# Performance work log

Hardware: AMD Instinct MI355X
Metric: run time of the kernel (lower is better)

## Reference

```python
import jax, jax.numpy as jnp
import numpy as np
import math

L, E, H, F, V, ML, B, S = 6, 1024, 16, 4096, 1024, 1024, 4, 1024
PAD = V - 1


def setup_inputs() -> dict:
    key = jax.random.key(0)
    ks = jax.random.split(key, 16)
    sc = 0.02
    nrm = lambda k, sh: jax.random.normal(k, sh, jnp.float32) * sc
    return dict(
        sequences=jax.random.randint(ks[0], (B, S), 0, V - 1),
        embed=nrm(ks[1], (V, E)),
        pos_emb=nrm(ks[2], (1, ML + 2, E)),
        dist_emb=nrm(ks[3], (ML + 1, H)),
        in_w=nrm(ks[4], (L, 3 * E, E)), in_b=nrm(ks[5], (L, 3 * E)),
        out_w=nrm(ks[6], (L, E, E)), out_b=nrm(ks[7], (L, E)),
        ln1_g=jnp.ones((L, E)), ln1_b=jnp.zeros((L, E)),
        ff1_w=nrm(ks[8], (L, F, E)), ff1_b=nrm(ks[9], (L, F)),
        ff2_w=nrm(ks[10], (L, E, F)), ff2_b=nrm(ks[11], (L, E)),
        ln2_g=jnp.ones((L, E)), ln2_b=jnp.zeros((L, E)),
        lnf_g=jnp.ones((E,)), lnf_b=jnp.zeros((E,)),
        gen_w=nrm(ks[12], (V, E)), gen_b=jnp.zeros((V,)),
    )


def _layer_norm(h, g, b, eps=1e-5):
    m = h.mean(-1, keepdims=True)
    v = ((h - m) ** 2).mean(-1, keepdims=True)
    return (h - m) * jax.lax.rsqrt(v + eps) * g + b


def reference(sequences, embed, pos_emb, dist_emb, in_w, in_b, out_w, out_b,
              ln1_g, ln1_b, ff1_w, ff1_b, ff2_w, ff2_b, ln2_g, ln2_b,
              lnf_g, lnf_b, gen_w, gen_b):
    b_, s_ = sequences.shape
    dh = E // H
    # token embedding * sqrt(E) + learned positional embedding
    x = embed[sequences] * math.sqrt(E) + pos_emb[:, :s_]  # [B,S,E]
    # relative-distance attention bias, clamped at max_len
    idx = jnp.arange(s_)
    dist = jnp.minimum(jnp.abs(idx[None, :] - idx[:, None]), ML)  # [S,S]
    bias = dist_emb[dist].transpose(2, 0, 1)[None]  # [1,H,S,S]
    causal = idx[None, :] <= idx[:, None]  # lower-triangular allowed
    bias = jnp.where(causal[None, None], bias, -jnp.inf)
    # key padding mask (additive -inf on padded keys)
    kpm = (sequences == PAD)  # [B,S]
    bias = jnp.where(kpm[:, None, None, :], -jnp.inf, bias)  # [B,H,S,S]

    scale = 1.0 / math.sqrt(dh)
    for l in range(L):
        qkv = jnp.einsum('bse,fe->bsf', x, in_w[l]) + in_b[l]
        q, k, v = jnp.split(qkv, 3, axis=-1)
        q = q.reshape(b_, s_, H, dh).transpose(0, 2, 1, 3)
        k = k.reshape(b_, s_, H, dh).transpose(0, 2, 1, 3)
        v = v.reshape(b_, s_, H, dh).transpose(0, 2, 1, 3)
        scores = jnp.einsum('bhqd,bhkd->bhqk', q, k) * scale + bias
        att = jax.nn.softmax(scores, axis=-1)
        ctx = jnp.einsum('bhqk,bhkd->bhqd', att, v)
        ctx = ctx.transpose(0, 2, 1, 3).reshape(b_, s_, E)
        attn_out = jnp.einsum('bse,fe->bsf', ctx, out_w[l]) + out_b[l]
        x = _layer_norm(x + attn_out, ln1_g[l], ln1_b[l])  # post-norm
        h = jax.nn.gelu(jnp.einsum('bse,fe->bsf', x, ff1_w[l]) + ff1_b[l], approximate=False)
        h = jnp.einsum('bsf,ef->bse', h, ff2_w[l]) + ff2_b[l]
        x = _layer_norm(x + h, ln2_g[l], ln2_b[l])
    x = _layer_norm(x, lnf_g, lnf_b)  # final encoder norm
    logits = jnp.einsum('bse,ve->bsv', x, gen_w) + gen_b
    return logits
```

## Files before the change

### kernel.cpp

```cpp
#include <hip/hip_runtime.h>
#include <math.h>
#include <stdint.h>

constexpr int kL = 6;
constexpr int kE = 1024;
constexpr int kH = 16;
constexpr int kF = 4096;
constexpr int kV = 1024;
constexpr int kB = 4;
constexpr int kS = 1024;
constexpr int kRows = kB * kS;

typedef __bf16 bf16_t;
typedef __bf16 bf16x8 __attribute__((ext_vector_type(8)));
typedef __bf16 bf16x4 __attribute__((ext_vector_type(4)));
typedef float f32x4 __attribute__((ext_vector_type(4)));
typedef unsigned int u32x2 __attribute__((ext_vector_type(2)));

#define AS1 __attribute__((address_space(1)))
#define AS3 __attribute__((address_space(3)))

__device__ __forceinline__ void gload_lds16(const void* g, void* l) {
  __builtin_amdgcn_global_load_lds((const AS1 unsigned int*)g, (AS3 unsigned int*)l, 16, 0, 0);
}

__device__ __forceinline__ unsigned lds_u32(const void* p) {
  return (unsigned)(uintptr_t)p;
}

__device__ __forceinline__ float gelu_f(float x) {
  return 0.5f * x * (1.0f + erff(x * 0.70710678118654752440f));
}

template <int CTRL>
__device__ __forceinline__ float dppf(float v) {
  return __builtin_bit_cast(float, __builtin_amdgcn_update_dpp(
      __builtin_bit_cast(int, v), __builtin_bit_cast(int, v), CTRL, 0xF, 0xF, false));
}

__global__ void cast_kernel(const float* __restrict__ in, bf16_t* __restrict__ out, int n4) {
  const int stride = gridDim.x * blockDim.x;
  for (int i = blockIdx.x * blockDim.x + threadIdx.x; i < n4; i += stride) {
    const float4 v = *(const float4*)(in + (size_t)i * 4);
    bf16x4 o;
    o[0] = (bf16_t)v.x; o[1] = (bf16_t)v.y; o[2] = (bf16_t)v.z; o[3] = (bf16_t)v.w;
    *(bf16x4*)(out + (size_t)i * 4) = o;
  }
}

__global__ void embed_kernel(const int* __restrict__ seq, const float* __restrict__ emb,
                             const float* __restrict__ pos, float* __restrict__ x32,
                             bf16_t* __restrict__ xb) {
  const int r = blockIdx.x;
  const int s = r & 1023;
  const int tok = seq[r];
  const int c = threadIdx.x << 2;
  const float4 e = *(const float4*)(emb + (size_t)tok * kE + c);
  const float4 pz = *(const float4*)(pos + (size_t)s * kE + c);
  float4 v;
  v.x = e.x * 32.0f + pz.x;
  v.y = e.y * 32.0f + pz.y;
  v.z = e.z * 32.0f + pz.z;
  v.w = e.w * 32.0f + pz.w;
  *(float4*)(x32 + (size_t)r * kE + c) = v;
  bf16x4 o;
  o[0] = (bf16_t)v.x; o[1] = (bf16_t)v.y; o[2] = (bf16_t)v.z; o[3] = (bf16_t)v.w;
  *(bf16x4*)(xb + (size_t)r * kE + c) = o;
}

template <int MODE>
__global__ void addln_kernel(float* __restrict__ x32, const void* __restrict__ res,
                             const float* __restrict__ gg, const float* __restrict__ bb,
                             bf16_t* __restrict__ xb, const float* __restrict__ bias2) {
  __shared__ float red[8];
  const int r = blockIdx.x;
  const int c = threadIdx.x << 2;
  float4 v = *(const float4*)(x32 + (size_t)r * kE + c);
  if (MODE == 0) {
    const bf16x4 t = *(const bf16x4*)((const bf16_t*)res + (size_t)r * kE + c);
    v.x += (float)t[0]; v.y += (float)t[1]; v.z += (float)t[2]; v.w += (float)t[3];
  }
  if (MODE == 2) {
    const bf16_t* p = (const bf16_t*)res;
#pragma unroll
    for (int part = 0; part < 4; ++part) {
      const bf16x4 t = *(const bf16x4*)(p + (size_t)part * kRows * kE + (size_t)r * kE + c);
      v.x += (float)t[0]; v.y += (float)t[1]; v.z += (float)t[2]; v.w += (float)t[3];
    }
    const float4 b2 = *(const float4*)(bias2 + c);
    v.x += b2.x; v.y += b2.y; v.z += b2.z; v.w += b2.w;
  }
  float s = v.x + v.y + v.z + v.w;
  float q = v.x * v.x + v.y * v.y + v.z * v.z + v.w * v.w;
#pragma unroll
  for (int off = 32; off >= 1; off >>= 1) {
    s += __shfl_xor(s, off, 64);
    q += __shfl_xor(q, off, 64);
  }
  const int w = threadIdx.x >> 6, lane = threadIdx.x & 63;
  if (lane == 0) { red[w] = s; red[4 + w] = q; }
  __syncthreads();
  s = red[0] + red[1] + red[2] + red[3];
  q = red[4] + red[5] + red[6] + red[7];
  const float mean = s * (1.0f / 1024.0f);
  const float var = q * (1.0f / 1024.0f) - mean * mean;
  const float rstd = rsqrtf(var + 1e-5f);
  const float4 g4 = *(const float4*)(gg + c);
  const float4 b4 = *(const float4*)(bb + c);
  float4 o;
  o.x = (v.x - mean) * rstd * g4.x + b4.x;
  o.y = (v.y - mean) * rstd * g4.y + b4.y;
  o.z = (v.z - mean) * rstd * g4.z + b4.z;
  o.w = (v.w - mean) * rstd * g4.w + b4.w;
  if (MODE != 1) *(float4*)(x32 + (size_t)r * kE + c) = o;
  bf16x4 ob;
  ob[0] = (bf16_t)o.x; ob[1] = (bf16_t)o.y; ob[2] = (bf16_t)o.z; ob[3] = (bf16_t)o.w;
  *(bf16x4*)(xb + (size_t)r * kE + c) = ob;
}

template <int EPI>
__launch_bounds__(256, 4)
__global__ void gemm128_kernel(const bf16_t* __restrict__ A, const bf16_t* __restrict__ Bt,
                               const float* __restrict__ bias, void* __restrict__ Cv,
                               int ldA, int ldB, int ldC, int kc, size_t zstride) {
  __shared__ bf16_t lA[64 * 64];
  __shared__ bf16_t lB[64 * 64];
  const int tid = threadIdx.x;
  const int w = tid >> 6;
  const int lane = tid & 63;
  const int g = lane >> 4;
  const int lr = lane & 15;

  const int nwg = gridDim.x * gridDim.y;
  const int lin = blockIdx.y * gridDim.x + blockIdx.x;
  const int cpx = nwg >> 3;
  const int swz = (lin & 7) * cpx + (lin >> 3);
  const int bx = swz % gridDim.x, by = swz / gridDim.x;
  const int bm0 = by << 7;
  const int bn0 = bx << 7;
  const int k0 = blockIdx.z * kc;
  const int wm = (w >> 1) << 6;
  const int wn = (w & 1) << 6;

  const int ln8 = lane >> 3, l8 = lane & 7;
  const int pg = l8 ^ ln8;
  const int arow0 = (w << 5) + (ln8 << 1) + (pg >> 2);
  const int arow1 = arow0 + 16;
  const int kpo = (pg & 3) << 3;
  const bf16_t* srcA0 = A + (size_t)(bm0 + arow0) * ldA + k0 + kpo;
  const bf16_t* srcA1 = A + (size_t)(bm0 + arow1) * ldA + k0 + kpo;
  const bf16_t* srcB0 = Bt + (size_t)(bn0 + arow0) * ldB + k0 + kpo;
  const bf16_t* srcB1 = Bt + (size_t)(bn0 + arow1) * ldB + k0 + kpo;
  bf16_t* dA0 = lA + (w << 10);
  bf16_t* dA1 = lA + (w << 10) + 512;
  bf16_t* dB0 = lB + (w << 10);
  bf16_t* dB1 = lB + (w << 10) + 512;

  f32x4 zz = {0.f, 0.f, 0.f, 0.f};
  f32x4 acc[4][4];
#pragma unroll
  for (int i = 0; i < 4; ++i)
#pragma unroll
    for (int j = 0; j < 4; ++j) acc[i][j] = zz;

  int paoff[4], pboff[4];
#pragma unroll
  for (int i = 0; i < 4; ++i) {
    const int ra = wm + i * 16 + lr;
    paoff[i] = ((ra >> 1) << 6) + (((((ra & 1) << 2) + g) ^ ((ra >> 1) & 7)) << 3);
    const int rb = wn + i * 16 + lr;
    pboff[i] = ((rb >> 1) << 6) + (((((rb & 1) << 2) + g) ^ ((rb >> 1) & 7)) << 3);
  }

  const int NT = kc >> 5;
  for (int t = 0; t < NT; ++t) {
    gload_lds16(srcA0, dA0);
    gload_lds16(srcA1, dA1);
    gload_lds16(srcB0, dB0);
    gload_lds16(srcB1, dB1);
    srcA0 += 32; srcA1 += 32; srcB0 += 32; srcB1 += 32;
    __syncthreads();
    bf16x8 a[4], b[4];
#pragma unroll
    for (int i = 0; i < 4; ++i) a[i] = *(const bf16x8*)&lA[paoff[i]];
#pragma unroll
    for (int i = 0; i < 4; ++i) b[i] = *(const bf16x8*)&lB[pboff[i]];
#pragma unroll
    for (int i = 0; i < 4; ++i)
#pragma unroll
      for (int j = 0; j < 4; ++j)
        acc[i][j] = __builtin_amdgcn_mfma_f32_16x16x32_bf16(a[i], b[j], acc[i][j], 0, 0, 0);
    __syncthreads();
  }

  bf16_t* outb = (bf16_t*)Cv;
  if (EPI == 3) outb += (size_t)blockIdx.z * zstride;
#pragma unroll
  for (int i = 0; i < 4; ++i) {
#pragma unroll
    for (int j = 0; j < 4; ++j) {
      const int col = bn0 + wn + j * 16 + lr;
      float bv = 0.0f;
      if (EPI != 3) bv = bias[col];
#pragma unroll
      for (int rg = 0; rg < 4; ++rg) {
        const int row = bm0 + wm + i * 16 + g * 4 + rg;
        float v = acc[i][j][rg] + bv;
        if (EPI == 2) v = gelu_f(v);
        if (EPI == 1) {
          ((float*)Cv)[(size_t)row * ldC + col] = v;
        } else {
          outb[(size_t)row * ldC + col] = (bf16_t)v;
        }
      }
    }
  }
}

__launch_bounds__(256, 3)
__global__ void attn_kernel(const bf16_t* __restrict__ qkv, const int* __restrict__ seq,
                            const float* __restrict__ dist_emb, bf16_t* __restrict__ ctx) {
  __shared__ float sbias[1024];
  __shared__ unsigned char spad[1024];
  __shared__ bf16_t kbuf[2][64 * 64];
  __shared__ bf16_t vbuf[2][4096];
  __shared__ bf16_t pbuf[4][16][72];
  const int tid = threadIdx.x;
  const int w = tid >> 6, lane = tid & 63, g = lane >> 4, lr = lane & 15;
  const int bid = blockIdx.x;
  const int qt = 15 - (bid >> 6);
  const int h = bid & 15, b = (bid >> 4) & 3;

  const int q0 = qt * 64 + w * 16;
  const bf16_t* qp = qkv + ((size_t)(b * kS + q0 + lr)) * 3072 + h * 64;

  const int p = (w * 64 + lane) * 16;
  const int s_kv = ((p >> 11) << 4) + ((p >> 5) & 15);
  const int s_dv = (((p >> 9) & 3) << 4) + ((p & 31) >> 1);
  const bf16_t* vsrc0 = qkv + ((size_t)(b * kS + s_kv)) * 3072 + 2048 + h * 64 + s_dv;

  const int klrow = (w << 3) + (lane >> 3);
  const int kscol = ((lane & 7) ^ (lane >> 3)) << 3;
  const bf16_t* ksrc0 = qkv + ((size_t)(b * kS + klrow)) * 3072 + 1024 + h * 64 + kscol;

  const int cs0k = (g ^ (lr & 7)) << 3;
  const int cs1k = ((4 + g) ^ (lr & 7)) << 3;

  const int* seqb = seq + b * kS;
  const int nt = qt + 1;

#define STAGEKV(bufi, kt_) {                                                        \
    gload_lds16(ksrc0 + (size_t)((kt_) * 64) * 3072, &kbuf[bufi][(w << 3) * 64]);   \
    gload_lds16(ksrc0 + (size_t)((kt_) * 64 + 32) * 3072,                           \
                &kbuf[bufi][(32 + (w << 3)) * 64]);                                 \
    gload_lds16(vsrc0 + (size_t)((kt_) * 64) * 3072, &vbuf[bufi][w << 9]);          \
    gload_lds16(vsrc0 + (size_t)((kt_) * 64 + 32) * 3072,                           \
                &vbuf[bufi][2048 + (w << 9)]);                                      \
  }

  STAGEKV(0, 0);
  const bf16x8 qf0 = *(const bf16x8*)(qp + g * 8);
  const bf16x8 qf1 = *(const bf16x8*)(qp + 32 + g * 8);
  for (int i = tid; i < 1024; i += 256) {
    sbias[i] = dist_emb[i * kH + h];
    spad[i] = (seqb[i] == kV - 1) ? 1 : 0;
  }

  f32x4 zz = {0.f, 0.f, 0.f, 0.f};
  f32x4 oacc[4];
#pragma unroll
  for (int n = 0; n < 4; ++n) oacc[n] = zz;
  float m_[4], l_[4];
#pragma unroll
  for (int j = 0; j < 4; ++j) { m_[j] = -1e30f; l_[j] = 0.f; }

  __syncthreads();

#define ATT_STEP64(kt_, bz) do {                                                    \
    bf16x8 kf0[4], kf1[4];                                                          \
    _Pragma("unroll")                                                               \
    for (int ns = 0; ns < 4; ++ns) {                                                \
      const int krow = (ns * 16 + lr) * 64;                                         \
      kf0[ns] = *(const bf16x8*)&kbuf[bz][krow + cs0k];                             \
      kf1[ns] = *(const bf16x8*)&kbuf[bz][krow + cs1k];                             \
    }                                                                               \
    f32x4 s_[4];                                                                    \
    _Pragma("unroll")                                                               \
    for (int ns = 0; ns < 4; ++ns) {                                                \
      f32x4 z = zz;                                                                 \
      z = __builtin_amdgcn_mfma_f32_16x16x32_bf16(qf0, kf0[ns], z, 0, 0, 0);        \
      z = __builtin_amdgcn_mfma_f32_16x16x32_bf16(qf1, kf1[ns], z, 0, 0, 0);        \
      s_[ns] = z;                                                                   \
    }                                                                               \
    const int colb = (kt_) * 64 + lr;                                               \
    bool pad[4];                                                                    \
    _Pragma("unroll")                                                               \
    for (int ns = 0; ns < 4; ++ns) pad[ns] = spad[colb + ns * 16] != 0;             \
    float sv[4][4], lmax[4];                                                        \
    _Pragma("unroll")                                                               \
    for (int j = 0; j < 4; ++j) {                                                   \
      const int r = q0 + g * 4 + j;                                                 \
      _Pragma("unroll")                                                             \
      for (int ns = 0; ns < 4; ++ns) {                                              \
        const int cc = colb + ns * 16;                                              \
        sv[ns][j] = (cc <= r && !pad[ns]) ? s_[ns][j] * 0.125f + sbias[r - cc]      \
                                          : -1e30f;                                 \
      }                                                                             \
      lmax[j] = fmaxf(fmaxf(sv[0][j], sv[1][j]), fmaxf(sv[2][j], sv[3][j]));        \
    }                                                                               \
             \
    const bool okk = (lmax[0] <= m_[0] + 8.0f) && (lmax[1] <= m_[1] + 8.0f) &&      \
                     (lmax[2] <= m_[2] + 8.0f) && (lmax[3] <= m_[3] + 8.0f);        \
    if (!__all((int)okk)) {                                                         \
      float mj[4], corr[4];                                                         \
      _Pragma("unroll")                                                             \
      for (int j = 0; j < 4; ++j) {                                                 \
        mj[j] = lmax[j];                                                            \
        mj[j] = fmaxf(mj[j], dppf<0x121>(mj[j]));                                   \
        mj[j] = fmaxf(mj[j], dppf<0x122>(mj[j]));                                   \
        mj[j] = fmaxf(mj[j], dppf<0x124>(mj[j]));                                   \
        mj[j] = fmaxf(mj[j], dppf<0x128>(mj[j]));                                   \
        const float mn = fmaxf(m_[j], mj[j]);                                       \
        corr[j] = __expf(m_[j] - mn);                                               \
        m_[j] = mn;                                                                 \
        l_[j] *= corr[j];                                                           \
      }                                                                             \
      _Pragma("unroll")                                                             \
      for (int n = 0; n < 4; ++n) {                                                 \
        f32x4 t = oacc[n];                                                          \
        t[0] *= corr[0]; t[1] *= corr[1]; t[2] *= corr[2]; t[3] *= corr[3];         \
        oacc[n] = t;                                                                \
      }                                                                             \
    }                                                                               \
    float pv[4][4];                                                                 \
    _Pragma("unroll")                                                               \
    for (int j = 0; j < 4; ++j) {                                                   \
      _Pragma("unroll")                                                             \
      for (int ns = 0; ns < 4; ++ns) pv[ns][j] = __expf(sv[ns][j] - m_[j]);         \
      l_[j] += (pv[0][j] + pv[1][j]) + (pv[2][j] + pv[3][j]);  \
    }                                                                               \
    _Pragma("unroll")                                                               \
    for (int j = 0; j < 4; ++j) {                                                   \
      _Pragma("unroll")                                                             \
      for (int ns = 0; ns < 4; ++ns)                                                \
        pbuf[w][g * 4 + j][ns * 16 + lr] = (bf16_t)pv[ns][j];                       \
    }                                                                               \
    asm volatile("s_waitcnt lgkmcnt(0)" ::: "memory");                              \
    const bf16x4 pa0 = *(const bf16x4*)&pbuf[w][lr][g * 4];                         \
    const bf16x4 pa1 = *(const bf16x4*)&pbuf[w][lr][16 + g * 4];                    \
    const bf16x4 pa2 = *(const bf16x4*)&pbuf[w][lr][32 + g * 4];                    \
    const bf16x4 pa3 = *(const bf16x4*)&pbuf[w][lr][48 + g * 4];                    \
    bf16x8 pfl, pfh;                                                                \
    _Pragma("unroll")                                                               \
    for (int j = 0; j < 4; ++j) {                                                   \
      pfl[j] = pa0[j]; pfl[4 + j] = pa1[j];                                         \
      pfh[j] = pa2[j]; pfh[4 + j] = pa3[j];                                         \
    }                                                                               \
    const unsigned vb0 = lds_u32(&vbuf[bz][0]) + g * 128 + lr * 8;                  \
    u32x2 vt[8], vth[8];                                                            \
    _Pragma("unroll")                                                               \
    for (int n = 0; n < 4; ++n) {                                                   \
      asm volatile("ds_read_b64_tr_b16 %0, %2\n\t"                                  \
                   "ds_read_b64_tr_b16 %1, %2 offset:2048"                          \
                   : "=&v"(vt[n * 2]), "=&v"(vt[n * 2 + 1])                         \
                   : "v"(vb0 + n * 512)                                             \
                   : "memory");                                                     \
      asm volatile("ds_read_b64_tr_b16 %0, %2 offset:4096\n\t"                      \
                   "ds_read_b64_tr_b16 %1, %2 offset:6144"                          \
                   : "=&v"(vth[n * 2]), "=&v"(vth[n * 2 + 1])                       \
                   : "v"(vb0 + n * 512)                                             \
                   : "memory");                                                     \
    }                                                                               \
    asm volatile("s_waitcnt lgkmcnt(0)" ::: "memory");                              \
    __builtin_amdgcn_sched_barrier(0);                                              \
    _Pragma("unroll")                                                               \
    for (int n = 0; n < 4; ++n) {                                                   \
      const bf16x4 v0 = __builtin_bit_cast(bf16x4, vt[n * 2]);                      \
      const bf16x4 v1 = __builtin_bit_cast(bf16x4, vt[n * 2 + 1]);                  \
      bf16x8 vf;                                                                    \
      _Pragma("unroll")                                                             \
      for (int j = 0; j < 4; ++j) { vf[j] = v0[j]; vf[4 + j] = v1[j]; }             \
      oacc[n] = __builtin_amdgcn_mfma_f32_16x16x32_bf16(pfl, vf, oacc[n], 0, 0, 0); \
      const bf16x4 h0 = __builtin_bit_cast(bf16x4, vth[n * 2]);                     \
      const bf16x4 h1 = __builtin_bit_cast(bf16x4, vth[n * 2 + 1]);                 \
      bf16x8 vfh;                                                                   \
      _Pragma("unroll")                                                             \
      for (int j = 0; j < 4; ++j) { vfh[j] = h0[j]; vfh[4 + j] = h1[j]; }           \
      oacc[n] = __builtin_amdgcn_mfma_f32_16x16x32_bf16(pfh, vfh, oacc[n], 0, 0, 0);\
    }                                                                               \
  } while (0)

  for (int kt = 0; kt < nt; kt += 2) {
    if (kt + 1 < nt) STAGEKV(1, kt + 1);
    ATT_STEP64(kt, 0);
    __syncthreads();
    if (kt + 2 < nt) STAGEKV(0, kt + 2);
    if (kt + 1 < nt) ATT_STEP64(kt + 1, 1);
    __syncthreads();
  }
#undef ATT_STEP64
#undef STAGEKV

#pragma unroll
  for (int j = 0; j < 4; ++j) {
    l_[j] += dppf<0x121>(l_[j]);
    l_[j] += dppf<0x122>(l_[j]);
    l_[j] += dppf<0x124>(l_[j]);
    l_[j] += dppf<0x128>(l_[j]);
  }
#pragma unroll
  for (int j = 0; j < 4; ++j) {
    const float inv = 1.0f / l_[j];
    const int r = q0 + g * 4 + j;
    bf16_t* dst = ctx + ((size_t)(b * kS + r)) * kE + h * 64;
#pragma unroll
    for (int n = 0; n < 4; ++n) dst[n * 16 + lr] = (bf16_t)(oacc[n][j] * inv);
  }
}

extern "C" void kernel_launch(void* const* d_in, const int* in_sizes, int n_in,
                              void* d_out, int out_size, void* d_ws, size_t ws_size,
                              hipStream_t stream) {
  (void)in_sizes; (void)n_in; (void)out_size;
  const int* seq = (const int*)d_in[0];
  const float* emb = (const float*)d_in[1];
  const float* pos = (const float*)d_in[2];
  const float* dist = (const float*)d_in[3];
  const float* in_w = (const float*)d_in[4];
  const float* in_b = (const float*)d_in[5];
  const float* out_w = (const float*)d_in[6];
  const float* out_b = (const float*)d_in[7];
  const float* ln1g = (const float*)d_in[8];
  const float* ln1b = (const float*)d_in[9];
  const float* ff1w = (const float*)d_in[10];
  const float* ff1b = (const float*)d_in[11];
  const float* ff2w = (const float*)d_in[12];
  const float* ff2b = (const float*)d_in[13];
  const float* ln2g = (const float*)d_in[14];
  const float* ln2b = (const float*)d_in[15];
  const float* lnfg = (const float*)d_in[16];
  const float* lnfb = (const float*)d_in[17];
  const float* genw = (const float*)d_in[18];
  const float* genb = (const float*)d_in[19];

  char* ws = (char*)d_ws;
  size_t off = 0;
  auto alloc = [&](size_t elems, size_t esz) -> void* {
    void* pp = ws + off;
    off += (elems * esz + 255) & ~(size_t)255;
    return pp;
  };
  bf16_t* w_in = (bf16_t*)alloc((size_t)kL * 3 * kE * kE, 2);
  bf16_t* w_out = (bf16_t*)alloc((size_t)kL * kE * kE, 2);
  bf16_t* w_f1 = (bf16_t*)alloc((size_t)kL * kF * kE, 2);
  bf16_t* w_f2 = (bf16_t*)alloc((size_t)kL * kE * kF, 2);
  bf16_t* w_g = (bf16_t*)alloc((size_t)kV * kE, 2);
  float* x32 = (float*)alloc((size_t)kRows * kE, 4);
  bf16_t* xb = (bf16_t*)alloc((size_t)kRows * kE, 2);
  bf16_t* qkvb = (bf16_t*)alloc((size_t)kRows * 3 * kE, 2);
  bf16_t* ctxb = (bf16_t*)alloc((size_t)kRows * kE, 2);
  bf16_t* tmp4 = (bf16_t*)alloc((size_t)4 * kRows * kE, 2);
  bf16_t* hb = (bf16_t*)alloc((size_t)kRows * kF, 2);
  if (off > ws_size) return;

  cast_kernel<<<2048, 256, 0, stream>>>(in_w, w_in, kL * 3 * kE * kE / 4);
  cast_kernel<<<2048, 256, 0, stream>>>(out_w, w_out, kL * kE * kE / 4);
  cast_kernel<<<2048, 256, 0, stream>>>(ff1w, w_f1, kL * kF * kE / 4);
  cast_kernel<<<2048, 256, 0, stream>>>(ff2w, w_f2, kL * kE * kF / 4);
  cast_kernel<<<1024, 256, 0, stream>>>(genw, w_g, kV * kE / 4);
  embed_kernel<<<kRows, 256, 0, stream>>>(seq, emb, pos, x32, xb);

  for (int l = 0; l < kL; ++l) {
    gemm128_kernel<0><<<dim3(3 * kE / 128, kRows / 128), 256, 0, stream>>>(
        xb, w_in + (size_t)l * 3 * kE * kE, in_b + (size_t)l * 3 * kE, qkvb,
        kE, kE, 3 * kE, kE, 0);
    attn_kernel<<<kB * kH * 16, 256, 0, stream>>>(qkvb, seq, dist, ctxb);
    gemm128_kernel<3><<<dim3(kE / 128, kRows / 128, 4), 256, 0, stream>>>(
        ctxb, w_out + (size_t)l * kE * kE, nullptr, tmp4,
        kE, kE, kE, 256, (size_t)kRows * kE);
    addln_kernel<2><<<kRows, 256, 0, stream>>>(x32, tmp4, ln1g + (size_t)l * kE,
                                               ln1b + (size_t)l * kE, xb, out_b + (size_t)l * kE);
    gemm128_kernel<2><<<dim3(kF / 128, kRows / 128), 256, 0, stream>>>(
        xb, w_f1 + (size_t)l * kF * kE, ff1b + (size_t)l * kF, hb,
        kE, kE, kF, kE, 0);
    gemm128_kernel<3><<<dim3(kE / 128, kRows / 128, 4), 256, 0, stream>>>(
        hb, w_f2 + (size_t)l * kE * kF, nullptr, tmp4,
        kF, kF, kE, kE, (size_t)kRows * kE);
    addln_kernel<2><<<kRows, 256, 0, stream>>>(x32, tmp4, ln2g + (size_t)l * kE,
                                               ln2b + (size_t)l * kE, xb, ff2b + (size_t)l * kE);
  }
  addln_kernel<1><<<kRows, 256, 0, stream>>>(x32, nullptr, lnfg, lnfb, xb, nullptr);
  gemm128_kernel<1><<<dim3(kV / 128, kRows / 128), 256, 0, stream>>>(
      xb, w_g, genb, (float*)d_out, kE, kE, kV, kE, 0);
}
```

Measured before the change: 1.388 ms.

## Give each wave private double-buffered LDS tiles and drop block barriers in GEMM

Each wave in the 128x128 GEMM now loads its own 64-row A and B slices into a private, double-buffered LDS region. It prefetches the next k-step while computing the current one and uses vmcnt waits in place of workgroup __syncthreads. This removes block-wide barrier stalls and overlaps global loads with MFMA work. The cost is that neighbouring waves load the same A/B rows twice, roughly doubling global load traffic, and LDS per block rises to 64KB, so launch bounds drop from 4 to 2 blocks per CU. The wave-private buffers also make correctness depend on each wave reading only data it loaded itself.

```diff
diff --git a/kernel.cpp b/kernel.cpp
--- a/kernel.cpp
+++ b/kernel.cpp
@@ -119,12 +119,11 @@
 }
 
 template <int EPI>
-__launch_bounds__(256, 4)
+__launch_bounds__(256, 2)
 __global__ void gemm128_kernel(const bf16_t* __restrict__ A, const bf16_t* __restrict__ Bt,
                                const float* __restrict__ bias, void* __restrict__ Cv,
                                int ldA, int ldB, int ldC, int kc, size_t zstride) {
-  __shared__ bf16_t lA[64 * 64];
-  __shared__ bf16_t lB[64 * 64];
+  __shared__ bf16_t lds[4][2][4096];
   const int tid = threadIdx.x;
   const int w = tid >> 6;
   const int lane = tid & 63;
@@ -144,17 +143,16 @@
 
   const int ln8 = lane >> 3, l8 = lane & 7;
   const int pg = l8 ^ ln8;
-  const int arow0 = (w << 5) + (ln8 << 1) + (pg >> 2);
-  const int arow1 = arow0 + 16;
+  const int rb_ = (ln8 << 1) + (pg >> 2);
   const int kpo = (pg & 3) << 3;
-  const bf16_t* srcA0 = A + (size_t)(bm0 + arow0) * ldA + k0 + kpo;
-  const bf16_t* srcA1 = A + (size_t)(bm0 + arow1) * ldA + k0 + kpo;
-  const bf16_t* srcB0 = Bt + (size_t)(bn0 + arow0) * ldB + k0 + kpo;
-  const bf16_t* srcB1 = Bt + (size_t)(bn0 + arow1) * ldB + k0 + kpo;
-  bf16_t* dA0 = lA + (w << 10);
-  bf16_t* dA1 = lA + (w << 10) + 512;
-  bf16_t* dB0 = lB + (w << 10);
-  bf16_t* dB1 = lB + (w << 10) + 512;
+  const bf16_t* sA0 = A + (size_t)(bm0 + wm + 0 + rb_) * ldA + k0 + kpo;
+  const bf16_t* sA1 = A + (size_t)(bm0 + wm + 16 + rb_) * ldA + k0 + kpo;
+  const bf16_t* sA2 = A + (size_t)(bm0 + wm + 32 + rb_) * ldA + k0 + kpo;
+  const bf16_t* sA3 = A + (size_t)(bm0 + wm + 48 + rb_) * ldA + k0 + kpo;
+  const bf16_t* sB0 = Bt + (size_t)(bn0 + wn + 0 + rb_) * ldB + k0 + kpo;
+  const bf16_t* sB1 = Bt + (size_t)(bn0 + wn + 16 + rb_) * ldB + k0 + kpo;
+  const bf16_t* sB2 = Bt + (size_t)(bn0 + wn + 32 + rb_) * ldB + k0 + kpo;
+  const bf16_t* sB3 = Bt + (size_t)(bn0 + wn + 48 + rb_) * ldB + k0 + kpo;
 
   f32x4 zz = {0.f, 0.f, 0.f, 0.f};
   f32x4 acc[4][4];
@@ -166,32 +164,50 @@
   int paoff[4], pboff[4];
 #pragma unroll
   for (int i = 0; i < 4; ++i) {
-    const int ra = wm + i * 16 + lr;
+    const int ra = i * 16 + lr;
     paoff[i] = ((ra >> 1) << 6) + (((((ra & 1) << 2) + g) ^ ((ra >> 1) & 7)) << 3);
-    const int rb = wn + i * 16 + lr;
-    pboff[i] = ((rb >> 1) << 6) + (((((rb & 1) << 2) + g) ^ ((rb >> 1) & 7)) << 3);
+    pboff[i] = 2048 + paoff[i];
+  }
+
+#define STAGE_W(bz_) {                                   \
+    gload_lds16(sA0, &lds[w][bz_][0]);                   \
+    gload_lds16(sA1, &lds[w][bz_][512]);                 \
+    gload_lds16(sA2, &lds[w][bz_][1024]);                \
+    gload_lds16(sA3, &lds[w][bz_][1536]);                \
+    gload_lds16(sB0, &lds[w][bz_][2048]);                \
+    gload_lds16(sB1, &lds[w][bz_][2560]);                \
+    gload_lds16(sB2, &lds[w][bz_][3072]);                \
+    gload_lds16(sB3, &lds[w][bz_][3584]);                \
+    sA0 += 32; sA1 += 32; sA2 += 32; sA3 += 32;          \
+    sB0 += 32; sB1 += 32; sB2 += 32; sB3 += 32;          \
   }
 
   const int NT = kc >> 5;
+  int bz = 0;
+  STAGE_W(0);
   for (int t = 0; t < NT; ++t) {
-    gload_lds16(srcA0, dA0);
-    gload_lds16(srcA1, dA1);
-    gload_lds16(srcB0, dB0);
-    gload_lds16(srcB1, dB1);
-    srcA0 += 32; srcA1 += 32; srcB0 += 32; srcB1 += 32;
-    __syncthreads();
+    if (t + 1 < NT) {
+      STAGE_W(bz ^ 1);
+      __builtin_amdgcn_sched_barrier(0);
+      asm volatile("s_waitcnt vmcnt(8)" ::: "memory");
+    } else {
+      __builtin_amdgcn_sched_barrier(0);
+      asm volatile("s_waitcnt vmcnt(0)" ::: "memory");
+    }
+    __builtin_amdgcn_sched_barrier(0);
     bf16x8 a[4], b[4];
 #pragma unroll
-    for (int i = 0; i < 4; ++i) a[i] = *(const bf16x8*)&lA[paoff[i]];
-#pragma unroll
-    for (int i = 0; i < 4; ++i) b[i] = *(const bf16x8*)&lB[pboff[i]];
+    for (int i = 0; i < 4; ++i) a[i] = *(const bf16x8*)&lds[w][bz][paoff[i]];
+#pragma unroll
+    for (int i = 0; i < 4; ++i) b[i] = *(const bf16x8*)&lds[w][bz][pboff[i]];
 #pragma unroll
     for (int i = 0; i < 4; ++i)
 #pragma unroll
       for (int j = 0; j < 4; ++j)
         acc[i][j] = __builtin_amdgcn_mfma_f32_16x16x32_bf16(a[i], b[j], acc[i][j], 0, 0, 0);
-    __syncthreads();
-  }
+    bz ^= 1;
+  }
+#undef STAGE_W
 
   bf16_t* outb = (bf16_t*)Cv;
   if (EPI == 3) outb += (size_t)blockIdx.z * zstride;
```

After: 1.705 ms. +22.9%, slower.
